# Kernel optimization log

Hardware: AMD Instinct MI355X
Metric: run time of the kernel (lower is better)

Reference implementation:

```python
import jax, jax.numpy as jnp
import numpy as np

DIM = 1024
NUM_HEADS = 16
HEAD_DIM = DIM // NUM_HEADS


def setup_inputs() -> dict:
    key = jax.random.key(0)
    k1, k2, k3, k4 = jax.random.split(key, 4)
    x = jax.random.normal(k1, (2, 2048, DIM), dtype=jnp.float32)
    # nn.Linear(dim, 3*dim, bias=False): weight [3*dim, dim], y = x @ W.T
    w_qkv = jax.random.normal(k2, (3 * DIM, DIM), dtype=jnp.float32) * (1.0 / np.sqrt(DIM))
    w_proj = jax.random.normal(k3, (DIM, DIM), dtype=jnp.float32) * (1.0 / np.sqrt(DIM))
    b_proj = jax.random.normal(k4, (DIM,), dtype=jnp.float32) * 0.02
    return {"x": x, "w_qkv": w_qkv, "w_proj": w_proj, "b_proj": b_proj}


def reference(x, w_qkv, w_proj, b_proj):
    B, N, C = x.shape
    H, D = NUM_HEADS, HEAD_DIM
    qkv = jnp.einsum('bnc,oc->bno', x, w_qkv)            # [B,N,3C]
    qkv = qkv.reshape(B, N, 3, H, D)
    q = jnp.transpose(qkv[:, :, 0], (0, 2, 1, 3))        # [B,H,N,D]
    k = jnp.transpose(qkv[:, :, 1], (0, 2, 1, 3))
    v = jnp.transpose(qkv[:, :, 2], (0, 2, 1, 3))
    scale = 1.0 / jnp.sqrt(jnp.asarray(D, dtype=x.dtype))
    scores = jnp.einsum('bhnd,bhmd->bhnm', q, k) * scale  # [B,H,N,N]
    attn = jax.nn.softmax(scores, axis=-1)
    o = jnp.einsum('bhnm,bhmd->bhnd', attn, v)            # [B,H,N,D]
    o = jnp.transpose(o, (0, 2, 1, 3)).reshape(B, N, C)
    return jnp.einsum('bnc,oc->bno', o, w_proj) + b_proj
```

## Files before the change

kernel.cpp:

```cpp
#include <hip/hip_runtime.h>
#include <cmath>

#define DIM 1024
#define NHEADS 16
#define HDIM 64
#define NB 2
#define SEQ 2048

typedef __bf16 bf16x8 __attribute__((ext_vector_type(8)));
typedef float f32x4 __attribute__((ext_vector_type(4)));

union Bf8 { bf16x8 v; __bf16 e[8]; unsigned short us[8]; };
union Bf1 { __bf16 b; unsigned short u; };

__device__ __forceinline__ void split_bf(float f, __bf16 &h, __bf16 &l) {
    h = (__bf16)f;
    l = (__bf16)(f - (float)h);
}
__device__ __forceinline__ unsigned int pack_bf(float f) {
    __bf16 h, l;
    split_bf(f, h, l);
    Bf1 ch, cl;
    ch.b = h; cl.b = l;
    return (unsigned int)ch.u | ((unsigned int)cl.u << 16);
}

template <bool HAS_BIAS>
__global__ __launch_bounds__(256) void gemm_nt_mfma(const float* __restrict__ A,
                                                    const float* __restrict__ W,
                                                    const float* __restrict__ bias,
                                                    float* __restrict__ C,
                                                    int M, int Nc, int K) {
    __shared__ __align__(16) __bf16 Ah[128][40];
    __shared__ __align__(16) __bf16 Al[128][40];
    __shared__ __align__(16) __bf16 Bh[128][40];
    __shared__ __align__(16) __bf16 Bl[128][40];

    const int nwg  = gridDim.x;
    const int orig = blockIdx.x;
    const int tile = (orig & 7) * (nwg >> 3) + (orig >> 3);
    const int gx   = Nc >> 7;
    const int m0   = (tile / gx) * 128;
    const int n0   = (tile % gx) * 128;

    const int t  = threadIdx.x;
    const int w  = t >> 6;
    const int l  = t & 63;
    const int wr = (w >> 1) * 64;
    const int wc = (w & 1) * 64;
    const int lr = l & 15;
    const int kg = l >> 4;

    const int srow = t >> 1;
    const int skh  = (t & 1) * 16;
    const float* Ap = A + (size_t)(m0 + srow) * K + skh;
    const float* Bp = W + (size_t)(n0 + srow) * K + skh;

    f32x4 acc[4][4] = {};

    for (int k0 = 0; k0 < K; k0 += 32) {
        float4 av[4], bv[4];
#pragma unroll
        for (int i = 0; i < 4; ++i) {
            av[i] = *reinterpret_cast<const float4*>(Ap + k0 + i * 4);
            bv[i] = *reinterpret_cast<const float4*>(Bp + k0 + i * 4);
        }
        __syncthreads();

#pragma unroll
        for (int half = 0; half < 2; ++half) {
            Bf8 vah, val_, vbh, vbl;
#pragma unroll
            for (int q = 0; q < 2; ++q) {
                const float4 va = av[half * 2 + q];
                const float4 vb = bv[half * 2 + q];
                const float fa[4] = {va.x, va.y, va.z, va.w};
                const float fb[4] = {vb.x, vb.y, vb.z, vb.w};
#pragma unroll
                for (int e = 0; e < 4; ++e) {
                    split_bf(fa[e], vah.e[q * 4 + e], val_.e[q * 4 + e]);
                    split_bf(fb[e], vbh.e[q * 4 + e], vbl.e[q * 4 + e]);
                }
            }
            *reinterpret_cast<bf16x8*>(&Ah[srow][skh + half * 8]) = vah.v;
            *reinterpret_cast<bf16x8*>(&Al[srow][skh + half * 8]) = val_.v;
            *reinterpret_cast<bf16x8*>(&Bh[srow][skh + half * 8]) = vbh.v;
            *reinterpret_cast<bf16x8*>(&Bl[srow][skh + half * 8]) = vbl.v;
        }
        __syncthreads();

        bf16x8 fah[4], fal[4], fbh[4], fbl[4];
#pragma unroll
        for (int mi = 0; mi < 4; ++mi) {
            fah[mi] = *reinterpret_cast<const bf16x8*>(&Ah[wr + mi * 16 + lr][kg * 8]);
            fal[mi] = *reinterpret_cast<const bf16x8*>(&Al[wr + mi * 16 + lr][kg * 8]);
        }
#pragma unroll
        for (int nj = 0; nj < 4; ++nj) {
            fbh[nj] = *reinterpret_cast<const bf16x8*>(&Bh[wc + nj * 16 + lr][kg * 8]);
            fbl[nj] = *reinterpret_cast<const bf16x8*>(&Bl[wc + nj * 16 + lr][kg * 8]);
        }
#pragma unroll
        for (int mi = 0; mi < 4; ++mi)
#pragma unroll
            for (int nj = 0; nj < 4; ++nj) {
                acc[mi][nj] = __builtin_amdgcn_mfma_f32_16x16x32_bf16(
                    fah[mi], fbh[nj], acc[mi][nj], 0, 0, 0);
                acc[mi][nj] = __builtin_amdgcn_mfma_f32_16x16x32_bf16(
                    fal[mi], fbh[nj], acc[mi][nj], 0, 0, 0);
                acc[mi][nj] = __builtin_amdgcn_mfma_f32_16x16x32_bf16(
                    fah[mi], fbl[nj], acc[mi][nj], 0, 0, 0);
            }
    }

    const int orow = kg * 4;
#pragma unroll
    for (int mi = 0; mi < 4; ++mi) {
#pragma unroll
        for (int r = 0; r < 4; ++r) {
            const int row = m0 + wr + mi * 16 + orow + r;
#pragma unroll
            for (int nj = 0; nj < 4; ++nj) {
                const int col = n0 + wc + nj * 16 + lr;
                float v = acc[mi][nj][r];
                if (HAS_BIAS) v += bias[col];
                C[(size_t)row * Nc + col] = v;
            }
        }
    }
}

__global__ __launch_bounds__(256, 2) void attn_mfma(const float* __restrict__ qkv,
                                                    float* __restrict__ o) {
    __shared__ __align__(16) __bf16 Khi[64][72];
    __shared__ __align__(16) __bf16 Klo[64][72];
    __shared__ __align__(16) __bf16 Vhi[64][72];
    __shared__ __align__(16) __bf16 Vlo[64][72];
    __shared__ __align__(16) unsigned int P32[128][68];

    const int nwg  = gridDim.x;
    const int orig = blockIdx.x;
    const int tile = (orig & 7) * (nwg >> 3) + (orig >> 3);
    const int qt = tile & 15;
    const int h  = (tile >> 4) & 15;
    const int b  = tile >> 8;

    const int t  = threadIdx.x;
    const int w  = t >> 6;
    const int l  = t & 63;
    const int lr = l & 15;
    const int kg = l >> 4;
    const int wq = w * 32;

    const size_t bbase = (size_t)b * SEQ * 3 * DIM;
    const int    hoff  = h * HDIM;

    bf16x8 qfh[2][2], qfl[2][2];
#pragma unroll
    for (int mi = 0; mi < 2; ++mi) {
#pragma unroll
        for (int ks = 0; ks < 2; ++ks) {
            const float* qp = qkv + bbase +
                (size_t)(qt * 128 + wq + mi * 16 + lr) * (3 * DIM) + hoff + ks * 32 + kg * 8;
            const float4 v0 = *reinterpret_cast<const float4*>(qp);
            const float4 v1 = *reinterpret_cast<const float4*>(qp + 4);
            const float f[8] = {v0.x, v0.y, v0.z, v0.w, v1.x, v1.y, v1.z, v1.w};
            Bf8 hh, ll;
#pragma unroll
            for (int e = 0; e < 8; ++e)
                split_bf(f[e] * 0.125f, hh.e[e], ll.e[e]);
            qfh[mi][ks] = hh.v;
            qfl[mi][ks] = ll.v;
        }
    }

    const int skey = t >> 2;
    const int sd0  = (t & 3) * 16;
    const int vkp  = (t & 31) * 2;
    const int vd0  = (t >> 5) * 8;

    const float* kptr  = qkv + bbase + DIM + hoff + (size_t)skey * (3 * DIM) + sd0;
    const float* vptr0 = qkv + bbase + 2 * DIM + hoff + (size_t)(vkp + 0) * (3 * DIM) + vd0;
    const float* vptr1 = qkv + bbase + 2 * DIM + hoff + (size_t)(vkp + 1) * (3 * DIM) + vd0;
    const size_t kvstep = (size_t)64 * 3 * DIM;

    float4 kreg[4], vreg[4];
#pragma unroll
    for (int i = 0; i < 4; ++i) kreg[i] = *reinterpret_cast<const float4*>(kptr + i * 4);
    vreg[0] = *reinterpret_cast<const float4*>(vptr0);
    vreg[1] = *reinterpret_cast<const float4*>(vptr0 + 4);
    vreg[2] = *reinterpret_cast<const float4*>(vptr1);
    vreg[3] = *reinterpret_cast<const float4*>(vptr1 + 4);

    f32x4 oacc[2][4] = {};
    float mrow[2][4], lrow[2][4];
#pragma unroll
    for (int mi = 0; mi < 2; ++mi)
#pragma unroll
        for (int r = 0; r < 4; ++r) { mrow[mi][r] = -INFINITY; lrow[mi][r] = 0.f; }

    for (int kt = 0; kt < SEQ / 64; ++kt) {
        __syncthreads();

#pragma unroll
        for (int c = 0; c < 2; ++c) {
            Bf8 hh, ll;
#pragma unroll
            for (int q = 0; q < 2; ++q) {
                const float4 v = kreg[c * 2 + q];
                const float f[4] = {v.x, v.y, v.z, v.w};
#pragma unroll
                for (int e = 0; e < 4; ++e)
                    split_bf(f[e], hh.e[q * 4 + e], ll.e[q * 4 + e]);
            }
            *reinterpret_cast<bf16x8*>(&Khi[skey][sd0 + c * 8]) = hh.v;
            *reinterpret_cast<bf16x8*>(&Klo[skey][sd0 + c * 8]) = ll.v;
        }
        {
            const float f0[8] = {vreg[0].x, vreg[0].y, vreg[0].z, vreg[0].w,
                                 vreg[1].x, vreg[1].y, vreg[1].z, vreg[1].w};
            const float f1[8] = {vreg[2].x, vreg[2].y, vreg[2].z, vreg[2].w,
                                 vreg[3].x, vreg[3].y, vreg[3].z, vreg[3].w};
#pragma unroll
            for (int e = 0; e < 8; ++e) {
                __bf16 h0, l0, h1, l1;
                split_bf(f0[e], h0, l0);
                split_bf(f1[e], h1, l1);
                Bf1 a, c2;
                a.b = h0; c2.b = h1;
                *reinterpret_cast<unsigned int*>(&Vhi[vd0 + e][vkp]) =
                    (unsigned int)a.u | ((unsigned int)c2.u << 16);
                a.b = l0; c2.b = l1;
                *reinterpret_cast<unsigned int*>(&Vlo[vd0 + e][vkp]) =
                    (unsigned int)a.u | ((unsigned int)c2.u << 16);
            }
        }
        __syncthreads();

        if (kt < SEQ / 64 - 1) {
            const float* kp  = kptr  + (size_t)(kt + 1) * kvstep;
            const float* vp0 = vptr0 + (size_t)(kt + 1) * kvstep;
            const float* vp1 = vptr1 + (size_t)(kt + 1) * kvstep;
#pragma unroll
            for (int i = 0; i < 4; ++i) kreg[i] = *reinterpret_cast<const float4*>(kp + i * 4);
            vreg[0] = *reinterpret_cast<const float4*>(vp0);
            vreg[1] = *reinterpret_cast<const float4*>(vp0 + 4);
            vreg[2] = *reinterpret_cast<const float4*>(vp1);
            vreg[3] = *reinterpret_cast<const float4*>(vp1 + 4);
        }

        f32x4 sacc[2][4] = {};
#pragma unroll
        for (int ks = 0; ks < 2; ++ks) {
#pragma unroll
            for (int nj = 0; nj < 4; ++nj) {
                const bf16x8 kh = *reinterpret_cast<const bf16x8*>(&Khi[nj * 16 + lr][ks * 32 + kg * 8]);
                const bf16x8 kl = *reinterpret_cast<const bf16x8*>(&Klo[nj * 16 + lr][ks * 32 + kg * 8]);
#pragma unroll
                for (int mi = 0; mi < 2; ++mi) {
                    sacc[mi][nj] = __builtin_amdgcn_mfma_f32_16x16x32_bf16(qfh[mi][ks], kh, sacc[mi][nj], 0, 0, 0);
                    sacc[mi][nj] = __builtin_amdgcn_mfma_f32_16x16x32_bf16(qfl[mi][ks], kh, sacc[mi][nj], 0, 0, 0);
                    sacc[mi][nj] = __builtin_amdgcn_mfma_f32_16x16x32_bf16(qfh[mi][ks], kl, sacc[mi][nj], 0, 0, 0);
                }
            }
        }

#pragma unroll
        for (int mi = 0; mi < 2; ++mi) {
#pragma unroll
            for (int r = 0; r < 4; ++r) {
                const float s0 = sacc[mi][0][r], s1 = sacc[mi][1][r];
                const float s2 = sacc[mi][2][r], s3 = sacc[mi][3][r];
                float pm = fmaxf(fmaxf(s0, s1), fmaxf(s2, s3));
                pm = fmaxf(pm, __shfl_xor(pm, 1));
                pm = fmaxf(pm, __shfl_xor(pm, 2));
                pm = fmaxf(pm, __shfl_xor(pm, 4));
                pm = fmaxf(pm, __shfl_xor(pm, 8));
                const float nm = fmaxf(mrow[mi][r], pm);
                const float p0 = __expf(s0 - nm), p1 = __expf(s1 - nm);
                const float p2 = __expf(s2 - nm), p3 = __expf(s3 - nm);
                float ls = (p0 + p1) + (p2 + p3);
                ls += __shfl_xor(ls, 1);
                ls += __shfl_xor(ls, 2);
                ls += __shfl_xor(ls, 4);
                ls += __shfl_xor(ls, 8);
                const float fac = __expf(mrow[mi][r] - nm);
                mrow[mi][r] = nm;
                lrow[mi][r] = lrow[mi][r] * fac + ls;
#pragma unroll
                for (int njd = 0; njd < 4; ++njd) oacc[mi][njd][r] *= fac;
                const int prow = wq + mi * 16 + kg * 4 + r;
                P32[prow][0 * 16 + lr] = pack_bf(p0);
                P32[prow][1 * 16 + lr] = pack_bf(p1);
                P32[prow][2 * 16 + lr] = pack_bf(p2);
                P32[prow][3 * 16 + lr] = pack_bf(p3);
            }
        }

#pragma unroll
        for (int ks = 0; ks < 2; ++ks) {
            bf16x8 ph[2], pl[2];
#pragma unroll
            for (int mi = 0; mi < 2; ++mi) {
                const unsigned int* pp = &P32[wq + mi * 16 + lr][ks * 32 + kg * 8];
                const uint4 u0 = *reinterpret_cast<const uint4*>(pp);
                const uint4 u1 = *reinterpret_cast<const uint4*>(pp + 4);
                const unsigned int uu[8] = {u0.x, u0.y, u0.z, u0.w, u1.x, u1.y, u1.z, u1.w};
                Bf8 hh, ll;
#pragma unroll
                for (int j = 0; j < 8; ++j) {
                    hh.us[j] = (unsigned short)(uu[j] & 0xffffu);
                    ll.us[j] = (unsigned short)(uu[j] >> 16);
                }
                ph[mi] = hh.v;
                pl[mi] = ll.v;
            }
#pragma unroll
            for (int njd = 0; njd < 4; ++njd) {
                const bf16x8 vh = *reinterpret_cast<const bf16x8*>(&Vhi[njd * 16 + lr][ks * 32 + kg * 8]);
                const bf16x8 vl = *reinterpret_cast<const bf16x8*>(&Vlo[njd * 16 + lr][ks * 32 + kg * 8]);
#pragma unroll
                for (int mi = 0; mi < 2; ++mi) {
                    oacc[mi][njd] = __builtin_amdgcn_mfma_f32_16x16x32_bf16(ph[mi], vh, oacc[mi][njd], 0, 0, 0);
                    oacc[mi][njd] = __builtin_amdgcn_mfma_f32_16x16x32_bf16(pl[mi], vh, oacc[mi][njd], 0, 0, 0);
                    oacc[mi][njd] = __builtin_amdgcn_mfma_f32_16x16x32_bf16(ph[mi], vl, oacc[mi][njd], 0, 0, 0);
                }
            }
        }
    }

#pragma unroll
    for (int mi = 0; mi < 2; ++mi) {
#pragma unroll
        for (int r = 0; r < 4; ++r) {
            const float inv = 1.f / lrow[mi][r];
            const int grow = b * SEQ + qt * 128 + wq + mi * 16 + kg * 4 + r;
#pragma unroll
            for (int njd = 0; njd < 4; ++njd)
                o[(size_t)grow * DIM + hoff + njd * 16 + lr] = oacc[mi][njd][r] * inv;
        }
    }
}

extern "C" void kernel_launch(void* const* d_in, const int* in_sizes, int n_in,
                              void* d_out, int out_size, void* d_ws, size_t ws_size,
                              hipStream_t stream) {
    const float* x      = (const float*)d_in[0];
    const float* w_qkv  = (const float*)d_in[1];
    const float* w_proj = (const float*)d_in[2];
    const float* b_proj = (const float*)d_in[3];
    float* out = (float*)d_out;

    const int M = NB * SEQ;
    float* qkv  = (float*)d_ws;
    float* obuf = qkv + (size_t)M * 3 * DIM;

    gemm_nt_mfma<false><<<dim3((M / 128) * (3 * DIM / 128)), 256, 0, stream>>>(
        x, w_qkv, nullptr, qkv, M, 3 * DIM, DIM);

    attn_mfma<<<dim3((SEQ / 128) * NHEADS * NB), 256, 0, stream>>>(qkv, obuf);

    gemm_nt_mfma<true><<<dim3((M / 128) * (DIM / 128)), 256, 0, stream>>>(
        obuf, w_proj, b_proj, out, M, DIM, DIM);
}
```

Before: 404.0 us.

## Store intermediates as pre-split bf16 hi/lo pairs instead of fp32

The QKV GEMM now writes its output as bf16 hi/lo pairs, with the Q scale folded into the epilogue. Attention reads those pairs directly, and the attention output is likewise stored split for the projection GEMM. This removes repeated per-tile fp32-to-bf16 splitting, which for K/V was redone by every query tile. When the workspace is large enough, x and both weight matrices are also pre-split by a separate kernel so the GEMMs load bf16 directly. The cost is three extra split kernels and extra workspace, and scattered 2-byte epilogue stores that may be poorly coalesced.

New measurement: 365.6 us. 1.1x faster.

```diff
diff --git a/kernel.cpp b/kernel.cpp
--- a/kernel.cpp
+++ b/kernel.cpp
@@ -8,10 +8,11 @@
 #define SEQ 2048
 
 typedef __bf16 bf16x8 __attribute__((ext_vector_type(8)));
+typedef __bf16 bf16x4 __attribute__((ext_vector_type(4)));
 typedef float f32x4 __attribute__((ext_vector_type(4)));
 
 union Bf8 { bf16x8 v; __bf16 e[8]; unsigned short us[8]; };
-union Bf1 { __bf16 b; unsigned short u; };
+union Bf4 { bf16x4 v; __bf16 e[4]; };
 
 __device__ __forceinline__ void split_bf(float f, __bf16 &h, __bf16 &l) {
     h = (__bf16)f;
@@ -20,17 +21,33 @@
 __device__ __forceinline__ unsigned int pack_bf(float f) {
     __bf16 h, l;
     split_bf(f, h, l);
-    Bf1 ch, cl;
+    union { __bf16 b; unsigned short u; } ch, cl;
     ch.b = h; cl.b = l;
     return (unsigned int)ch.u | ((unsigned int)cl.u << 16);
 }
 
-template <bool HAS_BIAS>
-__global__ __launch_bounds__(256) void gemm_nt_mfma(const float* __restrict__ A,
-                                                    const float* __restrict__ W,
-                                                    const float* __restrict__ bias,
-                                                    float* __restrict__ C,
-                                                    int M, int Nc, int K) {
+__global__ __launch_bounds__(256) void split_f32(const float* __restrict__ in,
+                                                 __bf16* __restrict__ hi,
+                                                 __bf16* __restrict__ lo, int n4) {
+    for (int i = blockIdx.x * blockDim.x + threadIdx.x; i < n4;
+         i += gridDim.x * blockDim.x) {
+        const float4 v = reinterpret_cast<const float4*>(in)[i];
+        const float f[4] = {v.x, v.y, v.z, v.w};
+        Bf4 h, l;
+#pragma unroll
+        for (int e = 0; e < 4; ++e) split_bf(f[e], h.e[e], l.e[e]);
+        reinterpret_cast<bf16x4*>(hi)[i] = h.v;
+        reinterpret_cast<bf16x4*>(lo)[i] = l.v;
+    }
+}
+
+template <bool SA, bool SB, bool SOUT, bool QSCALE, bool HAS_BIAS>
+__global__ __launch_bounds__(256) void gemm_nt_mfma(
+    const float* __restrict__ Af, const __bf16* __restrict__ Agh, const __bf16* __restrict__ Agl,
+    const float* __restrict__ Bf, const __bf16* __restrict__ Bgh, const __bf16* __restrict__ Bgl,
+    const float* __restrict__ bias,
+    float* __restrict__ Cf, __bf16* __restrict__ Cgh, __bf16* __restrict__ Cgl,
+    int M, int Nc, int K) {
     __shared__ __align__(16) __bf16 Ah[128][40];
     __shared__ __align__(16) __bf16 Al[128][40];
     __shared__ __align__(16) __bf16 Bh[128][40];
@@ -53,39 +70,77 @@
 
     const int srow = t >> 1;
     const int skh  = (t & 1) * 16;
-    const float* Ap = A + (size_t)(m0 + srow) * K + skh;
-    const float* Bp = W + (size_t)(n0 + srow) * K + skh;
+    const size_t arow = (size_t)(m0 + srow) * K + skh;
+    const size_t brow = (size_t)(n0 + srow) * K + skh;
 
     f32x4 acc[4][4] = {};
 
     for (int k0 = 0; k0 < K; k0 += 32) {
         float4 av[4], bv[4];
-#pragma unroll
-        for (int i = 0; i < 4; ++i) {
-            av[i] = *reinterpret_cast<const float4*>(Ap + k0 + i * 4);
-            bv[i] = *reinterpret_cast<const float4*>(Bp + k0 + i * 4);
+        bf16x8 sah[2], sal[2], sbh[2], sbl[2];
+        if constexpr (SA) {
+            sah[0] = *reinterpret_cast<const bf16x8*>(Agh + arow + k0);
+            sah[1] = *reinterpret_cast<const bf16x8*>(Agh + arow + k0 + 8);
+            sal[0] = *reinterpret_cast<const bf16x8*>(Agl + arow + k0);
+            sal[1] = *reinterpret_cast<const bf16x8*>(Agl + arow + k0 + 8);
+        } else {
+#pragma unroll
+            for (int i = 0; i < 4; ++i)
+                av[i] = *reinterpret_cast<const float4*>(Af + arow + k0 + i * 4);
+        }
+        if constexpr (SB) {
+            sbh[0] = *reinterpret_cast<const bf16x8*>(Bgh + brow + k0);
+            sbh[1] = *reinterpret_cast<const bf16x8*>(Bgh + brow + k0 + 8);
+            sbl[0] = *reinterpret_cast<const bf16x8*>(Bgl + brow + k0);
+            sbl[1] = *reinterpret_cast<const bf16x8*>(Bgl + brow + k0 + 8);
+        } else {
+#pragma unroll
+            for (int i = 0; i < 4; ++i)
+                bv[i] = *reinterpret_cast<const float4*>(Bf + brow + k0 + i * 4);
         }
         __syncthreads();
 
-#pragma unroll
-        for (int half = 0; half < 2; ++half) {
-            Bf8 vah, val_, vbh, vbl;
-#pragma unroll
-            for (int q = 0; q < 2; ++q) {
-                const float4 va = av[half * 2 + q];
-                const float4 vb = bv[half * 2 + q];
-                const float fa[4] = {va.x, va.y, va.z, va.w};
-                const float fb[4] = {vb.x, vb.y, vb.z, vb.w};
-#pragma unroll
-                for (int e = 0; e < 4; ++e) {
-                    split_bf(fa[e], vah.e[q * 4 + e], val_.e[q * 4 + e]);
-                    split_bf(fb[e], vbh.e[q * 4 + e], vbl.e[q * 4 + e]);
-                }
-            }
-            *reinterpret_cast<bf16x8*>(&Ah[srow][skh + half * 8]) = vah.v;
-            *reinterpret_cast<bf16x8*>(&Al[srow][skh + half * 8]) = val_.v;
-            *reinterpret_cast<bf16x8*>(&Bh[srow][skh + half * 8]) = vbh.v;
-            *reinterpret_cast<bf16x8*>(&Bl[srow][skh + half * 8]) = vbl.v;
+        if constexpr (SA) {
+            *reinterpret_cast<bf16x8*>(&Ah[srow][skh])     = sah[0];
+            *reinterpret_cast<bf16x8*>(&Ah[srow][skh + 8]) = sah[1];
+            *reinterpret_cast<bf16x8*>(&Al[srow][skh])     = sal[0];
+            *reinterpret_cast<bf16x8*>(&Al[srow][skh + 8]) = sal[1];
+        } else {
+#pragma unroll
+            for (int half = 0; half < 2; ++half) {
+                Bf8 hh, ll;
+#pragma unroll
+                for (int q = 0; q < 2; ++q) {
+                    const float4 va = av[half * 2 + q];
+                    const float fa[4] = {va.x, va.y, va.z, va.w};
+#pragma unroll
+                    for (int e = 0; e < 4; ++e)
+                        split_bf(fa[e], hh.e[q * 4 + e], ll.e[q * 4 + e]);
+                }
+                *reinterpret_cast<bf16x8*>(&Ah[srow][skh + half * 8]) = hh.v;
+                *reinterpret_cast<bf16x8*>(&Al[srow][skh + half * 8]) = ll.v;
+            }
+        }
+        if constexpr (SB) {
+            *reinterpret_cast<bf16x8*>(&Bh[srow][skh])     = sbh[0];
+            *reinterpret_cast<bf16x8*>(&Bh[srow][skh + 8]) = sbh[1];
+            *reinterpret_cast<bf16x8*>(&Bl[srow][skh])     = sbl[0];
+            *reinterpret_cast<bf16x8*>(&Bl[srow][skh + 8]) = sbl[1];
+        } else {
+#pragma unroll
+            for (int half = 0; half < 2; ++half) {
+                Bf8 hh, ll;
+#pragma unroll
+                for (int q = 0; q < 2; ++q) {
+                    const float4 vb = bv[half * 2 + q];
+                    const float fb[4] = {vb.x, vb.y, vb.z, vb.w};
+#pragma unroll
+                    for (int e = 0; e < 4; ++e)
+                        split_bf(fb[e], hh.e[q * 4 + e], ll.e[q * 4 + e]);
+                }
+                *reinterpret_cast<bf16x8*>(&Bh[srow][skh + half * 8]) = hh.v;
+                *reinterpret_cast<bf16x8*>(&Bl[srow][skh + half * 8]) = ll.v;
+            }
         }
         __syncthreads();
 
@@ -113,25 +168,38 @@
             }
     }
 
-    const int orow = kg * 4;
+    const int orw = kg * 4;
 #pragma unroll
     for (int mi = 0; mi < 4; ++mi) {
 #pragma unroll
         for (int r = 0; r < 4; ++r) {
-            const int row = m0 + wr + mi * 16 + orow + r;
+            const int row = m0 + wr + mi * 16 + orw + r;
 #pragma unroll
             for (int nj = 0; nj < 4; ++nj) {
                 const int col = n0 + wc + nj * 16 + lr;
                 float v = acc[mi][nj][r];
-                if (HAS_BIAS) v += bias[col];
-                C[(size_t)row * Nc + col] = v;
-            }
-        }
-    }
-}
-
-__global__ __launch_bounds__(256, 2) void attn_mfma(const float* __restrict__ qkv,
-                                                    float* __restrict__ o) {
+                if constexpr (SOUT) {
+                    if constexpr (QSCALE) {
+                        if (col < DIM) v *= 0.125f;
+                    }
+                    __bf16 hh, ll;
+                    split_bf(v, hh, ll);
+                    const size_t off = (size_t)row * Nc + col;
+                    Cgh[off] = hh;
+                    Cgl[off] = ll;
+                } else {
+                    if constexpr (HAS_BIAS) v += bias[col];
+                    Cf[(size_t)row * Nc + col] = v;
+                }
+            }
+        }
+    }
+}
+
+__global__ __launch_bounds__(256, 2) void attn_mfma(const __bf16* __restrict__ qkv_hi,
+                                                    const __bf16* __restrict__ qkv_lo,
+                                                    __bf16* __restrict__ o_hi,
+                                                    __bf16* __restrict__ o_lo) {
     __shared__ __align__(16) __bf16 Khi[64][72];
     __shared__ __align__(16) __bf16 Klo[64][72];
     __shared__ __align__(16) __bf16 Vhi[64][72];
@@ -160,17 +228,10 @@
     for (int mi = 0; mi < 2; ++mi) {
 #pragma unroll
         for (int ks = 0; ks < 2; ++ks) {
-            const float* qp = qkv + bbase +
+            const size_t qoff = bbase +
                 (size_t)(qt * 128 + wq + mi * 16 + lr) * (3 * DIM) + hoff + ks * 32 + kg * 8;
-            const float4 v0 = *reinterpret_cast<const float4*>(qp);
-            const float4 v1 = *reinterpret_cast<const float4*>(qp + 4);
-            const float f[8] = {v0.x, v0.y, v0.z, v0.w, v1.x, v1.y, v1.z, v1.w};
-            Bf8 hh, ll;
-#pragma unroll
-            for (int e = 0; e < 8; ++e)
-                split_bf(f[e] * 0.125f, hh.e[e], ll.e[e]);
-            qfh[mi][ks] = hh.v;
-            qfl[mi][ks] = ll.v;
+            qfh[mi][ks] = *reinterpret_cast<const bf16x8*>(qkv_hi + qoff);
+            qfl[mi][ks] = *reinterpret_cast<const bf16x8*>(qkv_lo + qoff);
         }
     }
 
@@ -179,18 +240,20 @@
     const int vkp  = (t & 31) * 2;
     const int vd0  = (t >> 5) * 8;
 
-    const float* kptr  = qkv + bbase + DIM + hoff + (size_t)skey * (3 * DIM) + sd0;
-    const float* vptr0 = qkv + bbase + 2 * DIM + hoff + (size_t)(vkp + 0) * (3 * DIM) + vd0;
-    const float* vptr1 = qkv + bbase + 2 * DIM + hoff + (size_t)(vkp + 1) * (3 * DIM) + vd0;
+    const size_t koff  = bbase + DIM + hoff + (size_t)skey * (3 * DIM) + sd0;
+    const size_t voff0 = bbase + 2 * DIM + hoff + (size_t)(vkp + 0) * (3 * DIM) + vd0;
+    const size_t voff1 = bbase + 2 * DIM + hoff + (size_t)(vkp + 1) * (3 * DIM) + vd0;
     const size_t kvstep = (size_t)64 * 3 * DIM;
 
-    float4 kreg[4], vreg[4];
-#pragma unroll
-    for (int i = 0; i < 4; ++i) kreg[i] = *reinterpret_cast<const float4*>(kptr + i * 4);
-    vreg[0] = *reinterpret_cast<const float4*>(vptr0);
-    vreg[1] = *reinterpret_cast<const float4*>(vptr0 + 4);
-    vreg[2] = *reinterpret_cast<const float4*>(vptr1);
-    vreg[3] = *reinterpret_cast<const float4*>(vptr1 + 4);
+    bf16x8 kr[4], vr[4];
+    kr[0] = *reinterpret_cast<const bf16x8*>(qkv_hi + koff);
+    kr[1] = *reinterpret_cast<const bf16x8*>(qkv_hi + koff + 8);
+    kr[2] = *reinterpret_cast<const bf16x8*>(qkv_lo + koff);
+    kr[3] = *reinterpret_cast<const bf16x8*>(qkv_lo + koff + 8);
+    vr[0] = *reinterpret_cast<const bf16x8*>(qkv_hi + voff0);
+    vr[1] = *reinterpret_cast<const bf16x8*>(qkv_hi + voff1);
+    vr[2] = *reinterpret_cast<const bf16x8*>(qkv_lo + voff0);
+    vr[3] = *reinterpret_cast<const bf16x8*>(qkv_lo + voff1);
 
     f32x4 oacc[2][4] = {};
     float mrow[2][4], lrow[2][4];
@@ -202,51 +265,35 @@
     for (int kt = 0; kt < SEQ / 64; ++kt) {
         __syncthreads();
 
-#pragma unroll
-        for (int c = 0; c < 2; ++c) {
-            Bf8 hh, ll;
-#pragma unroll
-            for (int q = 0; q < 2; ++q) {
-                const float4 v = kreg[c * 2 + q];
-                const float f[4] = {v.x, v.y, v.z, v.w};
-#pragma unroll
-                for (int e = 0; e < 4; ++e)
-                    split_bf(f[e], hh.e[q * 4 + e], ll.e[q * 4 + e]);
-            }
-            *reinterpret_cast<bf16x8*>(&Khi[skey][sd0 + c * 8]) = hh.v;
-            *reinterpret_cast<bf16x8*>(&Klo[skey][sd0 + c * 8]) = ll.v;
-        }
+        *reinterpret_cast<bf16x8*>(&Khi[skey][sd0])     = kr[0];
+        *reinterpret_cast<bf16x8*>(&Khi[skey][sd0 + 8]) = kr[1];
+        *reinterpret_cast<bf16x8*>(&Klo[skey][sd0])     = kr[2];
+        *reinterpret_cast<bf16x8*>(&Klo[skey][sd0 + 8]) = kr[3];
         {
-            const float f0[8] = {vreg[0].x, vreg[0].y, vreg[0].z, vreg[0].w,
-                                 vreg[1].x, vreg[1].y, vreg[1].z, vreg[1].w};
-            const float f1[8] = {vreg[2].x, vreg[2].y, vreg[2].z, vreg[2].w,
-                                 vreg[3].x, vreg[3].y, vreg[3].z, vreg[3].w};
+            Bf8 k0h, k1h, k0l, k1l;
+            k0h.v = vr[0]; k1h.v = vr[1]; k0l.v = vr[2]; k1l.v = vr[3];
 #pragma unroll
             for (int e = 0; e < 8; ++e) {
-                __bf16 h0, l0, h1, l1;
-                split_bf(f0[e], h0, l0);
-                split_bf(f1[e], h1, l1);
-                Bf1 a, c2;
-                a.b = h0; c2.b = h1;
                 *reinterpret_cast<unsigned int*>(&Vhi[vd0 + e][vkp]) =
-                    (unsigned int)a.u | ((unsigned int)c2.u << 16);
-                a.b = l0; c2.b = l1;
+                    (unsigned int)k0h.us[e] | ((unsigned int)k1h.us[e] << 16);
                 *reinterpret_cast<unsigned int*>(&Vlo[vd0 + e][vkp]) =
-                    (unsigned int)a.u | ((unsigned int)c2.u << 16);
+                    (unsigned int)k0l.us[e] | ((unsigned int)k1l.us[e] << 16);
             }
         }
         __syncthreads();
 
         if (kt < SEQ / 64 - 1) {
-            const float* kp  = kptr  + (size_t)(kt + 1) * kvstep;
-            const float* vp0 = vptr0 + (size_t)(kt + 1) * kvstep;
-            const float* vp1 = vptr1 + (size_t)(kt + 1) * kvstep;
-#pragma unroll
-            for (int i = 0; i < 4; ++i) kreg[i] = *reinterpret_cast<const float4*>(kp + i * 4);
-            vreg[0] = *reinterpret_cast<const float4*>(vp0);
-            vreg[1] = *reinterpret_cast<const float4*>(vp0 + 4);
-            vreg[2] = *reinterpret_cast<const float4*>(vp1);
-            vreg[3] = *reinterpret_cast<const float4*>(vp1 + 4);
+            const size_t kk = koff + (size_t)(kt + 1) * kvstep;
+            const size_t v0 = voff0 + (size_t)(kt + 1) * kvstep;
+            const size_t v1 = voff1 + (size_t)(kt + 1) * kvstep;
+            kr[0] = *reinterpret_cast<const bf16x8*>(qkv_hi + kk);
+            kr[1] = *reinterpret_cast<const bf16x8*>(qkv_hi + kk + 8);
+            kr[2] = *reinterpret_cast<const bf16x8*>(qkv_lo + kk);
+            kr[3] = *reinterpret_cast<const bf16x8*>(qkv_lo + kk + 8);
+            vr[0] = *reinterpret_cast<const bf16x8*>(qkv_hi + v0);
+            vr[1] = *reinterpret_cast<const bf16x8*>(qkv_hi + v1);
+            vr[2] = *reinterpret_cast<const bf16x8*>(qkv_lo + v0);
+            vr[3] = *reinterpret_cast<const bf16x8*>(qkv_lo + v1);
         }
 
         f32x4 sacc[2][4] = {};
@@ -336,8 +383,14 @@
             const float inv = 1.f / lrow[mi][r];
             const int grow = b * SEQ + qt * 128 + wq + mi * 16 + kg * 4 + r;
 #pragma unroll
-            for (int njd = 0; njd < 4; ++njd)
-                o[(size_t)grow * DIM + hoff + njd * 16 + lr] = oacc[mi][njd][r] * inv;
+            for (int njd = 0; njd < 4; ++njd) {
+                const float v = oacc[mi][njd][r] * inv;
+                __bf16 hh, ll;
+                split_bf(v, hh, ll);
+                const size_t off = (size_t)grow * DIM + hoff + njd * 16 + lr;
+                o_hi[off] = hh;
+                o_lo[off] = ll;
+            }
         }
     }
 }
@@ -352,14 +405,53 @@
     float* out = (float*)d_out;
 
     const int M = NB * SEQ;
-    float* qkv  = (float*)d_ws;
-    float* obuf = qkv + (size_t)M * 3 * DIM;
-
-    gemm_nt_mfma<false><<<dim3((M / 128) * (3 * DIM / 128)), 256, 0, stream>>>(
-        x, w_qkv, nullptr, qkv, M, 3 * DIM, DIM);
-
-    attn_mfma<<<dim3((SEQ / 128) * NHEADS * NB), 256, 0, stream>>>(qkv, obuf);
-
-    gemm_nt_mfma<true><<<dim3((M / 128) * (DIM / 128)), 256, 0, stream>>>(
-        obuf, w_proj, b_proj, out, M, DIM, DIM);
-}
+    const size_t qkvN  = (size_t)M * 3 * DIM;
+    const size_t obufN = (size_t)M * DIM;
+    const size_t xN    = (size_t)M * DIM;
+    const size_t wqN   = (size_t)(3 * DIM) * DIM;
+    const size_t wpN   = (size_t)DIM * DIM;
+
+    __bf16* p = (__bf16*)d_ws;
+    __bf16* qkv_hi = p;  p += qkvN;
+    __bf16* qkv_lo = p;  p += qkvN;
+    __bf16* ob_hi  = p;  p += obufN;
+    __bf16* ob_lo  = p;  p += obufN;
+    __bf16* x_hi   = p;  p += xN;
+    __bf16* x_lo   = p;  p += xN;
+    __bf16* wq_hi  = p;  p += wqN;
+    __bf16* wq_lo  = p;  p += wqN;
+    __bf16* wp_hi  = p;  p += wpN;
+    __bf16* wp_lo  = p;  p += wpN;
+    const size_t NEED_FULL = 2 * (qkvN + obufN + xN + wqN + wpN) * sizeof(__bf16);
+    const bool full = ws_size >= NEED_FULL;
+
+    if (full) {
+        split_f32<<<512, 256, 0, stream>>>(x,      x_hi,  x_lo,  (int)(xN / 4));
+        split_f32<<<512, 256, 0, stream>>>(w_qkv,  wq_hi, wq_lo, (int)(wqN / 4));
+        split_f32<<<256, 256, 0, stream>>>(w_proj, wp_hi, wp_lo, (int)(wpN / 4));
+        gemm_nt_mfma<true, true, true, true, false>
+            <<<dim3((M / 128) * (3 * DIM / 128)), 256, 0, stream>>>(
+            nullptr, x_hi, x_lo, nullptr, wq_hi, wq_lo,
+            nullptr, nullptr, qkv_hi, qkv_lo, M, 3 * DIM, DIM);
+    } else {
+        gemm_nt_mfma<false, false, true, true, false>
+            <<<dim3((M / 128) * (3 * DIM / 128)), 256, 0, stream>>>(
+            x, nullptr, nullptr, w_qkv, nullptr, nullptr,
+            nullptr, nullptr, qkv_hi, qkv_lo, M, 3 * DIM, DIM);
+    }
+
+    attn_mfma<<<dim3((SEQ / 128) * NHEADS * NB), 256, 0, stream>>>(
+        qkv_hi, qkv_lo, ob_hi, ob_lo);
+
+    if (full) {
+        gemm_nt_mfma<true, true, false, false, true>
+            <<<dim3((M / 128) * (DIM / 128)), 256, 0, stream>>>(
+            nullptr, ob_hi, ob_lo, nullptr, wp_hi, wp_lo,
+            b_proj, out, nullptr, nullptr, M, DIM, DIM);
+    } else {
+        gemm_nt_mfma<true, false, false, false, true>
+            <<<dim3((M / 128) * (DIM / 128)), 256, 0, stream>>>(
+            nullptr, ob_hi, ob_lo, w_proj, nullptr, nullptr,
+            b_proj, out, nullptr, nullptr, M, DIM, DIM);
+    }
+}
```
